# Optimization experiments

Hardware: AMD Instinct MI355X
Metric: run time of the kernel (lower is better)

The kernel has to match this reference:

```python
import jax, jax.numpy as jnp
import numpy as np

E = 8        # num_experts
TOP_K = 2    # num_experts_per_tok
H = 2048     # hidden_size
I = 1408     # moe_intermediate_size

def setup_inputs() -> dict:
    key = jax.random.key(0)
    k0, k1, k2, k3, k4 = jax.random.split(key, 5)
    hidden_states = jax.random.normal(k0, (2, 2048, H), dtype=jnp.float32)
    gate_w = jax.random.normal(k1, (E, H), dtype=jnp.float32) * 0.02   # router: Linear(H, E)
    wg = jax.random.normal(k2, (E, I, H), dtype=jnp.float32) * 0.02    # gate_proj per expert
    wu = jax.random.normal(k3, (E, I, H), dtype=jnp.float32) * 0.02    # up_proj per expert
    wd = jax.random.normal(k4, (E, H, I), dtype=jnp.float32) * 0.02    # down_proj per expert
    return {"hidden_states": hidden_states, "gate_w": gate_w, "wg": wg, "wu": wu, "wd": wd}

def reference(hidden_states, gate_w, wg, wu, wd):
    b, s, h = hidden_states.shape
    x = hidden_states.reshape(-1, h)                      # [T, H]
    router_logits = x @ gate_w.T                          # [T, E]
    routing_weights = jax.nn.softmax(router_logits.astype(jnp.float32), axis=-1)
    topk_weight, topk_idx = jax.lax.top_k(routing_weights, TOP_K)   # [T, K]
    topk_weight = topk_weight / jnp.sum(topk_weight, axis=-1, keepdims=True)
    # per-token combine weight for each expert: w[t,e] = sum_k topk_weight[t,k] * [topk_idx[t,k]==e]
    comb = jnp.sum(jax.nn.one_hot(topk_idx, E, dtype=x.dtype) * topk_weight[..., None].astype(x.dtype), axis=1)  # [T, E]
    # compute each expert on all tokens (dense faithful equivalent of masked dispatch), combine with comb
    def expert_out(e):
        g = x @ wg[e].T                                   # [T, I]
        u = x @ wu[e].T                                   # [T, I]
        return (jax.nn.silu(g) * u) @ wd[e].T             # [T, H]
    y = jnp.zeros_like(x)
    for e in range(E):  # small fixed expert count
        y = y + expert_out(e) * comb[:, e:e+1]
    final = y.reshape(b, s, h)
    return final, router_logits.astype(hidden_states.dtype)
```

## Files before the change

### kernel.cpp

```cpp
#include <hip/hip_runtime.h>

#define NTOK 4096
#define NEXP 8
#define HD 2048
#define ID 1408

typedef unsigned short u16;
typedef __attribute__((ext_vector_type(8))) short short8;
typedef __attribute__((ext_vector_type(4))) float f32x4;
typedef const __attribute__((address_space(1))) void* gas_ptr;
typedef __attribute__((address_space(3))) void* las_ptr;

__device__ __forceinline__ u16 f2bf(float f) {
  unsigned int u = __float_as_uint(f);
  u += 0x7FFFu + ((u >> 16) & 1u);
  return (u16)(u >> 16);
}

__device__ __forceinline__ void async16(const u16* g, u16* l) {
  __builtin_amdgcn_global_load_lds((gas_ptr)g, (las_ptr)l, 16, 0, 0);
}

__global__ void cvt_kernel(const float* __restrict__ s, u16* __restrict__ d, long n8) {
  long i = (long)blockIdx.x * blockDim.x + threadIdx.x;
  if (i >= n8) return;
  const float4* s4 = (const float4*)s;
  float4 a = s4[2*i], b = s4[2*i+1];
  short8 o;
  o[0] = (short)f2bf(a.x); o[1] = (short)f2bf(a.y);
  o[2] = (short)f2bf(a.z); o[3] = (short)f2bf(a.w);
  o[4] = (short)f2bf(b.x); o[5] = (short)f2bf(b.y);
  o[6] = (short)f2bf(b.z); o[7] = (short)f2bf(b.w);
  *(short8*)(d + 8*i) = o;
}

__global__ void router_kernel(const float* __restrict__ x, const float* __restrict__ gw,
                              float* __restrict__ logits, int* __restrict__ cnt,
                              int* __restrict__ ptok, float* __restrict__ pw) {
  int t = blockIdx.x * 4 + (threadIdx.x >> 6);
  int lane = threadIdx.x & 63;
  if (t >= NTOK) return;
  const float4* xr = (const float4*)(x + (size_t)t * HD);
  float dot[NEXP];
#pragma unroll
  for (int e = 0; e < NEXP; ++e) dot[e] = 0.f;
#pragma unroll
  for (int c = 0; c < 8; ++c) {
    float4 xv = xr[c*64 + lane];
#pragma unroll
    for (int e = 0; e < NEXP; ++e) {
      float4 gv = ((const float4*)(gw + e*HD))[c*64 + lane];
      dot[e] += xv.x*gv.x + xv.y*gv.y + xv.z*gv.z + xv.w*gv.w;
    }
  }
#pragma unroll
  for (int off = 32; off > 0; off >>= 1) {
#pragma unroll
    for (int e = 0; e < NEXP; ++e) dot[e] += __shfl_xor(dot[e], off);
  }
  if (lane < NEXP) logits[(size_t)t*NEXP + lane] = dot[lane];
  if (lane == 0) {
    float mx = dot[0];
#pragma unroll
    for (int e = 1; e < NEXP; ++e) mx = fmaxf(mx, dot[e]);
    float p[NEXP];
#pragma unroll
    for (int e = 0; e < NEXP; ++e) p[e] = __expf(dot[e] - mx);
    int e0 = 0;
#pragma unroll
    for (int e = 1; e < NEXP; ++e) if (p[e] > p[e0]) e0 = e;
    int e1 = (e0 == 0) ? 1 : 0;
#pragma unroll
    for (int e = 0; e < NEXP; ++e) if (e != e0 && p[e] > p[e1]) e1 = e;
    float denom = p[e0] + p[e1];
    int pos0 = atomicAdd(&cnt[e0], 1);
    ptok[e0*NTOK + pos0] = t; pw[e0*NTOK + pos0] = p[e0] / denom;
    int pos1 = atomicAdd(&cnt[e1], 1);
    ptok[e1*NTOK + pos1] = t; pw[e1*NTOK + pos1] = p[e1] / denom;
  }
}

__global__ void prefix_kernel(const int* __restrict__ cnt, int* __restrict__ offs) {
  if (threadIdx.x == 0) {
    int a = 0;
    for (int e = 0; e < NEXP; ++e) { offs[e] = a; a += cnt[e]; }
  }
}

__global__ __launch_bounds__(256, 2) void gemm1_kernel(
    const u16* __restrict__ xb, const u16* __restrict__ wgb, const u16* __restrict__ wub,
    const int* __restrict__ cnt, const int* __restrict__ offs,
    const int* __restrict__ ptok, u16* __restrict__ hbuf) {
  int e = blockIdx.z, mt = blockIdx.y, nt = blockIdx.x;
  int c = cnt[e];
  if (mt * 128 >= c) return;
  int off = offs[e];

  __shared__ u16 sA[128*32], sBg[128*32], sBu[128*32];

  int tid = threadIdx.x;
  int r0 = tid >> 2;
  int ch = (tid & 3) * 8;
  int s0 = mt*128 + r0, s1 = s0 + 64;
  int t0 = ptok[e*NTOK + (s0 < c ? s0 : 0)];
  int t1 = ptok[e*NTOK + (s1 < c ? s1 : 0)];
  const u16* ga0 = xb + (size_t)t0*HD + ch;
  const u16* ga1 = xb + (size_t)t1*HD + ch;
  int n0 = nt*128 + r0;
  const u16* gg0 = wgb + ((size_t)e*ID + n0)*HD + ch;
  const u16* gg1 = gg0 + (size_t)64*HD;
  const u16* gu0 = wub + ((size_t)e*ID + n0)*HD + ch;
  const u16* gu1 = gu0 + (size_t)64*HD;

  int lane = tid & 63, wv = tid >> 6, wr = wv >> 1, wc = wv & 1;
  int fm = lane & 15, kg = lane >> 4;

  f32x4 accg[4][4], accu[4][4];
#pragma unroll
  for (int i = 0; i < 4; ++i)
#pragma unroll
    for (int j = 0; j < 4; ++j) {
      accg[i][j] = {0.f, 0.f, 0.f, 0.f};
      accu[i][j] = {0.f, 0.f, 0.f, 0.f};
    }

  const u16* sAf  = sA  + (wr*64 + fm)*32 + kg*8;
  const u16* sBgf = sBg + (wc*64 + fm)*32 + kg*8;
  const u16* sBuf = sBu + (wc*64 + fm)*32 + kg*8;

  for (int k0 = 0; k0 < HD; k0 += 32) {
    async16(ga0 + k0, sA + tid*8);
    async16(ga1 + k0, sA + 2048 + tid*8);
    async16(gg0 + k0, sBg + tid*8);
    async16(gg1 + k0, sBg + 2048 + tid*8);
    async16(gu0 + k0, sBu + tid*8);
    async16(gu1 + k0, sBu + 2048 + tid*8);
    __syncthreads();
    short8 af[4], bg[4], bu[4];
#pragma unroll
    for (int i = 0; i < 4; ++i) af[i] = *(const short8*)(sAf + i*512);
#pragma unroll
    for (int j = 0; j < 4; ++j) {
      bg[j] = *(const short8*)(sBgf + j*512);
      bu[j] = *(const short8*)(sBuf + j*512);
    }
#pragma unroll
    for (int i = 0; i < 4; ++i)
#pragma unroll
      for (int j = 0; j < 4; ++j) {
        accg[i][j] = __builtin_amdgcn_mfma_f32_16x16x32_bf16(af[i], bg[j], accg[i][j], 0, 0, 0);
        accu[i][j] = __builtin_amdgcn_mfma_f32_16x16x32_bf16(af[i], bu[j], accu[i][j], 0, 0, 0);
      }
    __syncthreads();
  }

#pragma unroll
  for (int i = 0; i < 4; ++i) {
#pragma unroll
    for (int r = 0; r < 4; ++r) {
      int slot = mt*128 + wr*64 + i*16 + kg*4 + r;
      if (slot < c) {
        size_t rowb = (size_t)(off + slot) * ID + nt*128 + wc*64 + fm;
#pragma unroll
        for (int j = 0; j < 4; ++j) {
          float g = accg[i][j][r], u = accu[i][j][r];
          float hh = g * u / (1.f + __expf(-g));
          hbuf[rowb + (size_t)j*16] = f2bf(hh);
        }
      }
    }
  }
}

__global__ __launch_bounds__(256, 2) void gemm2_kernel(
    const u16* __restrict__ hbuf, const u16* __restrict__ wdb,
    const int* __restrict__ cnt, const int* __restrict__ offs,
    const int* __restrict__ ptok, const float* __restrict__ pw,
    float* __restrict__ out) {
  int e = blockIdx.z, mt = blockIdx.y, nt = blockIdx.x;
  int c = cnt[e];
  if (mt * 128 >= c) return;
  int off = offs[e];

  __shared__ u16 sA[128*32], sB[128*32];

  int tid = threadIdx.x;
  int r0 = tid >> 2;
  int ch = (tid & 3) * 8;
  int s0 = mt*128 + r0, s1 = s0 + 64;
  const u16* ga0 = hbuf + (size_t)(off + (s0 < c ? s0 : 0))*ID + ch;
  const u16* ga1 = hbuf + (size_t)(off + (s1 < c ? s1 : 0))*ID + ch;
  int n0 = nt*128 + r0;
  const u16* gb0 = wdb + ((size_t)e*HD + n0)*ID + ch;
  const u16* gb1 = gb0 + (size_t)64*ID;

  int lane = tid & 63, wv = tid >> 6, wr = wv >> 1, wc = wv & 1;
  int fm = lane & 15, kg = lane >> 4;

  f32x4 acc[4][4];
#pragma unroll
  for (int i = 0; i < 4; ++i)
#pragma unroll
    for (int j = 0; j < 4; ++j) acc[i][j] = {0.f, 0.f, 0.f, 0.f};

  const u16* sAf = sA + (wr*64 + fm)*32 + kg*8;
  const u16* sBf = sB + (wc*64 + fm)*32 + kg*8;

  for (int k0 = 0; k0 < ID; k0 += 32) {
    async16(ga0 + k0, sA + tid*8);
    async16(ga1 + k0, sA + 2048 + tid*8);
    async16(gb0 + k0, sB + tid*8);
    async16(gb1 + k0, sB + 2048 + tid*8);
    __syncthreads();
    short8 af[4], bf[4];
#pragma unroll
    for (int i = 0; i < 4; ++i) af[i] = *(const short8*)(sAf + i*512);
#pragma unroll
    for (int j = 0; j < 4; ++j) bf[j] = *(const short8*)(sBf + j*512);
#pragma unroll
    for (int i = 0; i < 4; ++i)
#pragma unroll
      for (int j = 0; j < 4; ++j)
        acc[i][j] = __builtin_amdgcn_mfma_f32_16x16x32_bf16(af[i], bf[j], acc[i][j], 0, 0, 0);
    __syncthreads();
  }

#pragma unroll
  for (int i = 0; i < 4; ++i) {
#pragma unroll
    for (int r = 0; r < 4; ++r) {
      int slot = mt*128 + wr*64 + i*16 + kg*4 + r;
      if (slot < c) {
        int tok = ptok[e*NTOK + slot];
        float wgt = pw[e*NTOK + slot];
        float* orow = out + (size_t)tok*HD + nt*128 + wc*64 + fm;
#pragma unroll
        for (int j = 0; j < 4; ++j)
          atomicAdd(orow + j*16, wgt * acc[i][j][r]);
      }
    }
  }
}

extern "C" void kernel_launch(void* const* d_in, const int* in_sizes, int n_in,
                              void* d_out, int out_size, void* d_ws, size_t ws_size,
                              hipStream_t stream) {
  const float* x  = (const float*)d_in[0];
  const float* gw = (const float*)d_in[1];
  const float* wg = (const float*)d_in[2];
  const float* wu = (const float*)d_in[3];
  const float* wd = (const float*)d_in[4];
  float* out = (float*)d_out;

  char* p = (char*)d_ws;
  u16*   xb   = (u16*)(p);
  u16*   wgb  = (u16*)(p + 16777216UL);
  u16*   wub  = (u16*)(p + 62914560UL);
  u16*   wdb  = (u16*)(p + 109051904UL);
  u16*   hbuf = (u16*)(p + 155189248UL);
  int*   ptok = (int*)(p + 178257920UL);
  float* pww  = (float*)(p + 178388992UL);
  int*   cnt  = (int*)(p + 178520064UL);
  int*   offs = (int*)(p + 178520320UL);

  hipMemsetAsync(out, 0, (size_t)NTOK * HD * sizeof(float), stream);
  hipMemsetAsync(cnt, 0, NEXP * sizeof(int), stream);

  cvt_kernel<<<4096, 256, 0, stream>>>(x, xb, (long)NTOK * HD / 8);
  cvt_kernel<<<11264, 256, 0, stream>>>(wg, wgb, (long)NEXP * ID * HD / 8);
  cvt_kernel<<<11264, 256, 0, stream>>>(wu, wub, (long)NEXP * ID * HD / 8);
  cvt_kernel<<<11264, 256, 0, stream>>>(wd, wdb, (long)NEXP * HD * ID / 8);

  router_kernel<<<1024, 256, 0, stream>>>(x, gw, out + (size_t)NTOK * HD, cnt, ptok, pww);
  prefix_kernel<<<1, 64, 0, stream>>>(cnt, offs);

  gemm1_kernel<<<dim3(11, 32, 8), 256, 0, stream>>>(xb, wgb, wub, cnt, offs, ptok, hbuf);
  gemm2_kernel<<<dim3(16, 32, 8), 256, 0, stream>>>(hbuf, wdb, cnt, offs, ptok, pww, out);
}
```

Measured before the change: 699.8 us.

## Fuse x conversion into router, replace atomic scatter with bf16 rank buffer and combine

The activation bf16 conversion now happens inside the router kernel, which removes one launch and one extra read of x. The second GEMM no longer zeroes the output and does float atomicAdds. Instead it writes weighted bf16 partial results into a per-token, per-rank buffer that reuses the xb workspace region, and a new combine kernel sums the two ranks into fp32. The grid axes are also swapped so that M tiles vary fastest, which may change L2 reuse of weight tiles. This trades atomic contention and the memset for extra bf16 rounding of the partials and an additional small pass.

```diff
diff --git a/kernel.cpp b/kernel.cpp
--- a/kernel.cpp
+++ b/kernel.cpp
@@ -7,6 +7,7 @@
 
 typedef unsigned short u16;
 typedef __attribute__((ext_vector_type(8))) short short8;
+typedef __attribute__((ext_vector_type(4))) unsigned short ushort4v;
 typedef __attribute__((ext_vector_type(4))) float f32x4;
 typedef const __attribute__((address_space(1))) void* gas_ptr;
 typedef __attribute__((address_space(3))) void* las_ptr;
@@ -16,7 +17,9 @@
   u += 0x7FFFu + ((u >> 16) & 1u);
   return (u16)(u >> 16);
 }
-
+__device__ __forceinline__ float bf2f(u16 b) {
+  return __uint_as_float(((unsigned int)b) << 16);
+}
 __device__ __forceinline__ void async16(const u16* g, u16* l) {
   __builtin_amdgcn_global_load_lds((gas_ptr)g, (las_ptr)l, 16, 0, 0);
 }
@@ -35,6 +38,7 @@
 }
 
 __global__ void router_kernel(const float* __restrict__ x, const float* __restrict__ gw,
+                              u16* __restrict__ xb,
                               float* __restrict__ logits, int* __restrict__ cnt,
                               int* __restrict__ ptok, float* __restrict__ pw) {
   int t = blockIdx.x * 4 + (threadIdx.x >> 6);
@@ -47,6 +51,9 @@
 #pragma unroll
   for (int c = 0; c < 8; ++c) {
     float4 xv = xr[c*64 + lane];
+    ushort4v o;
+    o[0] = f2bf(xv.x); o[1] = f2bf(xv.y); o[2] = f2bf(xv.z); o[3] = f2bf(xv.w);
+    *(ushort4v*)(xb + (size_t)t*HD + (c*64 + lane)*4) = o;
 #pragma unroll
     for (int e = 0; e < NEXP; ++e) {
       float4 gv = ((const float4*)(gw + e*HD))[c*64 + lane];
@@ -74,9 +81,11 @@
     for (int e = 0; e < NEXP; ++e) if (e != e0 && p[e] > p[e1]) e1 = e;
     float denom = p[e0] + p[e1];
     int pos0 = atomicAdd(&cnt[e0], 1);
-    ptok[e0*NTOK + pos0] = t; pw[e0*NTOK + pos0] = p[e0] / denom;
+    ptok[e0*NTOK + pos0] = t;
+    pw[e0*NTOK + pos0] = p[e0] / denom;
     int pos1 = atomicAdd(&cnt[e1], 1);
-    ptok[e1*NTOK + pos1] = t; pw[e1*NTOK + pos1] = p[e1] / denom;
+    ptok[e1*NTOK + pos1] = t | 0x10000;
+    pw[e1*NTOK + pos1] = p[e1] / denom;
   }
 }
 
@@ -91,7 +100,7 @@
     const u16* __restrict__ xb, const u16* __restrict__ wgb, const u16* __restrict__ wub,
     const int* __restrict__ cnt, const int* __restrict__ offs,
     const int* __restrict__ ptok, u16* __restrict__ hbuf) {
-  int e = blockIdx.z, mt = blockIdx.y, nt = blockIdx.x;
+  int e = blockIdx.z, mt = blockIdx.x, nt = blockIdx.y;
   int c = cnt[e];
   if (mt * 128 >= c) return;
   int off = offs[e];
@@ -102,8 +111,8 @@
   int r0 = tid >> 2;
   int ch = (tid & 3) * 8;
   int s0 = mt*128 + r0, s1 = s0 + 64;
-  int t0 = ptok[e*NTOK + (s0 < c ? s0 : 0)];
-  int t1 = ptok[e*NTOK + (s1 < c ? s1 : 0)];
+  int t0 = ptok[e*NTOK + (s0 < c ? s0 : 0)] & 0xFFFF;
+  int t1 = ptok[e*NTOK + (s1 < c ? s1 : 0)] & 0xFFFF;
   const u16* ga0 = xb + (size_t)t0*HD + ch;
   const u16* ga1 = xb + (size_t)t1*HD + ch;
   int n0 = nt*128 + r0;
@@ -176,8 +185,8 @@
     const u16* __restrict__ hbuf, const u16* __restrict__ wdb,
     const int* __restrict__ cnt, const int* __restrict__ offs,
     const int* __restrict__ ptok, const float* __restrict__ pw,
-    float* __restrict__ out) {
-  int e = blockIdx.z, mt = blockIdx.y, nt = blockIdx.x;
+    u16* __restrict__ ybuf) {
+  int e = blockIdx.z, mt = blockIdx.x, nt = blockIdx.y;
   int c = cnt[e];
   if (mt * 128 >= c) return;
   int off = offs[e];
@@ -231,15 +240,36 @@
     for (int r = 0; r < 4; ++r) {
       int slot = mt*128 + wr*64 + i*16 + kg*4 + r;
       if (slot < c) {
-        int tok = ptok[e*NTOK + slot];
+        int entry = ptok[e*NTOK + slot];
+        int tok = entry & 0xFFFF;
+        int rank = entry >> 16;
         float wgt = pw[e*NTOK + slot];
-        float* orow = out + (size_t)tok*HD + nt*128 + wc*64 + fm;
+        u16* orow = ybuf + ((size_t)tok*2 + rank)*HD + nt*128 + wc*64 + fm;
 #pragma unroll
         for (int j = 0; j < 4; ++j)
-          atomicAdd(orow + j*16, wgt * acc[i][j][r]);
+          orow[j*16] = f2bf(wgt * acc[i][j][r]);
       }
     }
   }
+}
+
+__global__ void combine_kernel(const u16* __restrict__ ybuf, float* __restrict__ out) {
+  int t = blockIdx.x;
+  int col = threadIdx.x * 8;
+  short8 a = *(const short8*)(ybuf + ((size_t)t*2)*HD + col);
+  short8 b = *(const short8*)(ybuf + ((size_t)t*2 + 1)*HD + col);
+  float4 o0, o1;
+  o0.x = bf2f((u16)a[0]) + bf2f((u16)b[0]);
+  o0.y = bf2f((u16)a[1]) + bf2f((u16)b[1]);
+  o0.z = bf2f((u16)a[2]) + bf2f((u16)b[2]);
+  o0.w = bf2f((u16)a[3]) + bf2f((u16)b[3]);
+  o1.x = bf2f((u16)a[4]) + bf2f((u16)b[4]);
+  o1.y = bf2f((u16)a[5]) + bf2f((u16)b[5]);
+  o1.z = bf2f((u16)a[6]) + bf2f((u16)b[6]);
+  o1.w = bf2f((u16)a[7]) + bf2f((u16)b[7]);
+  float4* dst = (float4*)(out + (size_t)t*HD + col);
+  dst[0] = o0;
+  dst[1] = o1;
 }
 
 extern "C" void kernel_launch(void* const* d_in, const int* in_sizes, int n_in,
@@ -253,6 +283,7 @@
   float* out = (float*)d_out;
 
   char* p = (char*)d_ws;
+  u16*   ybuf = (u16*)(p);
   u16*   xb   = (u16*)(p);
   u16*   wgb  = (u16*)(p + 16777216UL);
   u16*   wub  = (u16*)(p + 62914560UL);
@@ -263,17 +294,16 @@
   int*   cnt  = (int*)(p + 178520064UL);
   int*   offs = (int*)(p + 178520320UL);
 
-  hipMemsetAsync(out, 0, (size_t)NTOK * HD * sizeof(float), stream);
   hipMemsetAsync(cnt, 0, NEXP * sizeof(int), stream);
 
-  cvt_kernel<<<4096, 256, 0, stream>>>(x, xb, (long)NTOK * HD / 8);
   cvt_kernel<<<11264, 256, 0, stream>>>(wg, wgb, (long)NEXP * ID * HD / 8);
   cvt_kernel<<<11264, 256, 0, stream>>>(wu, wub, (long)NEXP * ID * HD / 8);
   cvt_kernel<<<11264, 256, 0, stream>>>(wd, wdb, (long)NEXP * HD * ID / 8);
 
-  router_kernel<<<1024, 256, 0, stream>>>(x, gw, out + (size_t)NTOK * HD, cnt, ptok, pww);
+  router_kernel<<<1024, 256, 0, stream>>>(x, gw, xb, out + (size_t)NTOK * HD, cnt, ptok, pww);
   prefix_kernel<<<1, 64, 0, stream>>>(cnt, offs);
 
-  gemm1_kernel<<<dim3(11, 32, 8), 256, 0, stream>>>(xb, wgb, wub, cnt, offs, ptok, hbuf);
-  gemm2_kernel<<<dim3(16, 32, 8), 256, 0, stream>>>(hbuf, wdb, cnt, offs, ptok, pww, out);
-}
+  gemm1_kernel<<<dim3(32, 11, 8), 256, 0, stream>>>(xb, wgb, wub, cnt, offs, ptok, hbuf);
+  gemm2_kernel<<<dim3(32, 16, 8), 256, 0, stream>>>(hbuf, wdb, cnt, offs, ptok, pww, ybuf);
+  combine_kernel<<<NTOK, 256, 0, stream>>>(ybuf, out);
+}
```

Result: slower. 1.020 ms (+45.7%).
